# Performance work log

Hardware: AMD Instinct MI355X
Metric: run time of the kernel (lower is better)

Reference implementation:

```python
import jax, jax.numpy as jnp
import numpy as np

HEADS = 8
DIM_HEAD = 64
EPS = 1e-4
SCALE = DIM_HEAD ** -0.5


def setup_inputs() -> dict:
    key = jax.random.key(0)
    k1, k2, k3, k4 = jax.random.split(key, 4)
    dim = HEADS * DIM_HEAD  # 512
    x = jax.random.normal(k1, (2, 2048, dim), dtype=jnp.float32)
    # torch Linear weights are [out, in]; scale like default init
    Wq = jax.random.normal(k2, (dim, dim), dtype=jnp.float32) / np.sqrt(dim)
    Wkv = jax.random.normal(k3, (2 * dim, dim), dtype=jnp.float32) / np.sqrt(dim)
    Wout = jax.random.normal(k4, (dim, dim), dtype=jnp.float32) / np.sqrt(dim)
    return {"x": x, "Wq": Wq, "Wkv": Wkv, "Wout": Wout}


def _normalize_magnitude(t, eps=EPS):
    # divide by (sqrt(mean(t^2, -1)) + eps)
    mag = jnp.sqrt(jnp.mean(t * t, axis=-1, keepdims=True)) + eps
    return t / mag


def reference(x, Wq, Wkv, Wout):
    b, n, dim = x.shape
    h, d = HEADS, DIM_HEAD
    # norm=False -> Identity; context = x (self-attention)
    q = x @ Wq.T                      # [b, n, h*d]
    kv = x @ Wkv.T                    # [b, n, 2*h*d]
    k, v = jnp.split(kv, 2, axis=-1)
    def to_heads(t):
        return t.reshape(b, n, h, d).transpose(0, 2, 1, 3)  # [b, h, n, d]
    q, k, v = map(to_heads, (q, k, v))
    q = _normalize_magnitude(q)
    k = _normalize_magnitude(k)
    sim = jnp.einsum('bhid,bhjd->bhij', q, k) * SCALE
    attn = jax.nn.softmax(sim, axis=-1)
    out = jnp.einsum('bhij,bhjd->bhid', attn, v)
    out = out.transpose(0, 2, 1, 3).reshape(b, n, h * d)
    return out @ Wout.T
```

## Files before the change

### kernel.cpp

```cpp
#include <hip/hip_runtime.h>

typedef __bf16 bf16x8 __attribute__((ext_vector_type(8)));
typedef __bf16 bf16x4 __attribute__((ext_vector_type(4)));
typedef float  f32x4  __attribute__((ext_vector_type(4)));

#define LOG2E_F 1.44269504088896340736f

static constexpr int kB = 2, kN = 2048, kH = 8, kD = 64, kDim = 512;
static constexpr int kTok = kB * kN;
static constexpr int kNQKV = 1536;
static constexpr int kKH = 4;

__device__ __forceinline__ void gld16(const void* g, void* l) {
  __builtin_amdgcn_global_load_lds(
      (const __attribute__((address_space(1))) void*)g,
      (__attribute__((address_space(3))) void*)l, 16, 0, 0);
}


__global__ __launch_bounds__(256) void cvt_all(const float* __restrict__ x,
                                               const float* __restrict__ wq,
                                               const float* __restrict__ wkv,
                                               const float* __restrict__ wo,
                                               __bf16* __restrict__ xb,
                                               __bf16* __restrict__ wqkvb,
                                               __bf16* __restrict__ wob) {
  size_t i = ((size_t)blockIdx.x * 256 + threadIdx.x) * 8;
  const float* s; __bf16* d; size_t off;
  if (i < 2097152)      { s = x;   d = xb;              off = i; }
  else if (i < 2359296) { s = wq;  d = wqkvb;           off = i - 2097152; }
  else if (i < 2883584) { s = wkv; d = wqkvb + 262144;  off = i - 2359296; }
  else                  { s = wo;  d = wob;             off = i - 2883584; }
  float4 u = *(const float4*)(s + off);
  float4 v = *(const float4*)(s + off + 4);
  bf16x8 t;
  t[0] = (__bf16)u.x; t[1] = (__bf16)u.y; t[2] = (__bf16)u.z; t[3] = (__bf16)u.w;
  t[4] = (__bf16)v.x; t[5] = (__bf16)v.y; t[6] = (__bf16)v.z; t[7] = (__bf16)v.w;
  *(bf16x8*)(d + off) = t;
}

__global__ __launch_bounds__(256, 2) void gemm_qkv(const __bf16* __restrict__ A,
                                                   const __bf16* __restrict__ B,
                                                   __bf16* __restrict__ qn,
                                                   __bf16* __restrict__ kn,
                                                   __bf16* __restrict__ vt2) {
  const int K = kDim;
  const int tid = threadIdx.x;
  const int w = tid >> 6, lane = tid & 63, quad = lane >> 4, lq = lane & 15;
  const int m0 = blockIdx.y * 128;
  const int n0 = blockIdx.x * 128;
  const int wm = (w >> 1) * 64, wn = (w & 1) * 64;
  __shared__ __bf16 shm[32768];

  const f32x4 zero = {0.f, 0.f, 0.f, 0.f};
  f32x4 acc[4][4];
#pragma unroll
  for (int fm = 0; fm < 4; ++fm)
#pragma unroll
    for (int fn = 0; fn < 4; ++fn) acc[fm][fn] = zero;

  auto stage = [&](int k0, int buf) {
#pragma unroll
    for (int j = 0; j < 4; ++j) {
      const int s = j * 256 + tid;
      const int row = s >> 3, ch = s & 7;
      const int off = k0 + ((ch ^ (row & 7)) << 3);
      gld16(A + (size_t)(m0 + row) * K + off, &shm[buf * 8192 + s * 8]);
      gld16(B + (size_t)(n0 + row) * K + off, &shm[16384 + buf * 8192 + s * 8]);
    }
  };
  const int sw0 = ((quad ^ (lq & 7)) << 3);
  const int sw1 = (((4 | quad) ^ (lq & 7)) << 3);

  stage(0, 0);
  for (int i = 0; i < 8; ++i) {
    __syncthreads();
    if (i < 7) stage((i + 1) << 6, (i + 1) & 1);
    const int ab = (i & 1) * 8192;
#pragma unroll
    for (int ks = 0; ks < 2; ++ks) {
      const int sw = ks ? sw1 : sw0;
      bf16x8 a[4], b[4];
#pragma unroll
      for (int fm = 0; fm < 4; ++fm)
        a[fm] = *(const bf16x8*)&shm[ab + (wm + fm * 16 + lq) * 64 + sw];
#pragma unroll
      for (int fn = 0; fn < 4; ++fn)
        b[fn] = *(const bf16x8*)&shm[16384 + ab + (wn + fn * 16 + lq) * 64 + sw];
#pragma unroll
      for (int fm = 0; fm < 4; ++fm)
#pragma unroll
        for (int fn = 0; fn < 4; ++fn)
          acc[fm][fn] =
              __builtin_amdgcn_mfma_f32_16x16x32_bf16(a[fm], b[fn], acc[fm][fn], 0, 0, 0);
    }
  }

  const int nb = n0 + wn;
  if (n0 >= 1024) {
    __syncthreads();
    const int hh = wn >> 6;
    const int b = m0 >> 11, kt0 = (m0 & (kN - 1)) >> 6;
#pragma unroll
    for (int fm = 0; fm < 4; ++fm)
#pragma unroll
      for (int r = 0; r < 4; ++r) {
        const int mo = wm + fm * 16 + quad * 4 + r;
        const int rh = mo >> 6, tt = mo & 63;
        const int p = (tt & 15) * 4 + (tt >> 4);
#pragma unroll
        for (int fn = 0; fn < 4; ++fn)
          shm[(hh * 2 + rh) * 4608 + (fn * 16 + lq) * 72 + p] = (__bf16)acc[fm][fn][r];
      }
    __syncthreads();
    const int dd = tid >> 2, p0 = (tid & 3) << 4;
    const int hbase = (n0 >> 6) & 7;
#pragma unroll
    for (int t = 0; t < 4; ++t) {
      const __bf16* src = &shm[t * 4608 + dd * 72 + p0];
      __bf16* dst = vt2 +
          ((size_t)((b * kH + hbase + (t >> 1)) * 32 + kt0 + (t & 1))) * 4096 + tid * 16;
      *(bf16x8*)dst = *(const bf16x8*)src;
      *(bf16x8*)(dst + 8) = *(const bf16x8*)(src + 8);
    }
  } else {
    const int h = (nb >> 6) & 7;
    const float qs = (nb < 512) ? (0.125f * LOG2E_F) : 1.0f;
    __bf16* dst0 = (nb < 512) ? qn : kn;
#pragma unroll
    for (int fm = 0; fm < 4; ++fm)
#pragma unroll
      for (int r = 0; r < 4; ++r) {
        float ss = 0.f;
#pragma unroll
        for (int fn = 0; fn < 4; ++fn) ss += acc[fm][fn][r] * acc[fm][fn][r];
#pragma unroll
        for (int off = 1; off < 16; off <<= 1) ss += __shfl_xor(ss, off, 64);
        const float inv = qs / (sqrtf(ss * (1.f / 64)) + 1e-4f);
        const int m = m0 + wm + fm * 16 + quad * 4 + r;
        const int b = m >> 11, n = m & (kN - 1);
        __bf16* dst = dst0 + ((size_t)(b * kH + h) * kN + n) * kD;
#pragma unroll
        for (int fn = 0; fn < 4; ++fn)
          dst[fn * 16 + lq] = (__bf16)(acc[fm][fn][r] * inv);
      }
  }
}

__global__ __launch_bounds__(256, 2) void attn(const __bf16* __restrict__ qn,
                                               const __bf16* __restrict__ kn,
                                               const __bf16* __restrict__ vt2,
                                               __bf16* __restrict__ po,
                                               float* __restrict__ pl) {
  const int qt = blockIdx.x, bh = blockIdx.y, kh = blockIdx.z;
  const int tid = threadIdx.x;
  const int w = tid >> 6, lane = tid & 63, quad = lane >> 4, lq = lane & 15;
  __shared__ __bf16 Ks[2][4096];
  __shared__ __bf16 Vs[2][4096];
  __shared__ __bf16 Ps[4][64 * 72];
  __bf16* myP = &Ps[w][0];

  bf16x8 aq[4][2];
#pragma unroll
  for (int fm = 0; fm < 4; ++fm) {
    const __bf16* Qb = qn + ((size_t)bh * kN + qt * 256 + w * 64 + fm * 16 + lq) * kD;
    aq[fm][0] = *(const bf16x8*)(Qb + quad * 8);
    aq[fm][1] = *(const bf16x8*)(Qb + 32 + quad * 8);
  }

  const f32x4 zero  = {0.f, 0.f, 0.f, 0.f};
  const f32x4 minit = {-12.f, -12.f, -12.f, -12.f};
  f32x4 o[4][4];
  float lr[4][4];
#pragma unroll
  for (int fm = 0; fm < 4; ++fm)
#pragma unroll
    for (int i = 0; i < 4; ++i) { o[fm][i] = zero; lr[fm][i] = 0.f; }

  const __bf16* Kb = kn + (size_t)bh * kN * kD;
  const __bf16* Vb = vt2 + (size_t)bh * 32 * 4096;

  auto stage = [&](int ktg, int buf) {
#pragma unroll
    for (int j = 0; j < 2; ++j) {
      const int s = j * 256 + tid;
      const int row = s >> 3, ch = s & 7;
      const int src = row * 64 + ((ch ^ (row & 7)) << 3);
      gld16(Kb + (size_t)ktg * 4096 + src, &Ks[buf][s * 8]);
      gld16(Vb + (size_t)ktg * 4096 + src, &Vs[buf][s * 8]);
    }
  };
  const int sw0 = ((quad ^ (lq & 7)) << 3);
  const int sw1 = (((4 | quad) ^ (lq & 7)) << 3);

  const int kt0 = kh * 8;
  stage(kt0, 0);
  for (int kt = 0; kt < 8; ++kt) {
    __syncthreads();
    if (kt < 7) stage(kt0 + kt + 1, (kt + 1) & 1);
    const __bf16* ks_ = &Ks[kt & 1][0];
    const __bf16* vs_ = &Vs[kt & 1][0];

    bf16x8 kb0[4], kb1[4];
#pragma unroll
    for (int fn = 0; fn < 4; ++fn) {
      const int rb = (fn * 16 + lq) * 64;
      kb0[fn] = *(const bf16x8*)&ks_[rb + sw0];
      kb1[fn] = *(const bf16x8*)&ks_[rb + sw1];
    }
#pragma unroll
    for (int fm = 0; fm < 4; ++fm) {
      f32x4 s[4];
#pragma unroll
      for (int fn = 0; fn < 4; ++fn) {
        f32x4 a = __builtin_amdgcn_mfma_f32_16x16x32_bf16(aq[fm][0], kb0[fn], minit, 0, 0, 0);
        s[fn] = __builtin_amdgcn_mfma_f32_16x16x32_bf16(aq[fm][1], kb1[fn], a, 0, 0, 0);
      }
#pragma unroll
      for (int r = 0; r < 4; ++r) {
        const float p0 = __builtin_amdgcn_exp2f(s[0][r]);
        const float p1 = __builtin_amdgcn_exp2f(s[1][r]);
        const float p2 = __builtin_amdgcn_exp2f(s[2][r]);
        const float p3 = __builtin_amdgcn_exp2f(s[3][r]);
        lr[fm][r] += (p0 + p1) + (p2 + p3);
        bf16x4 pk = {(__bf16)p0, (__bf16)p1, (__bf16)p2, (__bf16)p3};
        *(bf16x4*)&myP[(fm * 16 + quad * 4 + r) * 72 + lq * 4] = pk;
      }
    }
    bf16x8 vb0[4], vb1[4];
#pragma unroll
    for (int fn = 0; fn < 4; ++fn) {
      const int rb = (fn * 16 + lq) * 64;
      vb0[fn] = *(const bf16x8*)&vs_[rb + sw0];
      vb1[fn] = *(const bf16x8*)&vs_[rb + sw1];
    }
#pragma unroll
    for (int fm = 0; fm < 4; ++fm) {
      bf16x8 ap0 = *(const bf16x8*)&myP[(fm * 16 + lq) * 72 + quad * 8];
      bf16x8 ap1 = *(const bf16x8*)&myP[(fm * 16 + lq) * 72 + 32 + quad * 8];
#pragma unroll
      for (int fn = 0; fn < 4; ++fn) {
        o[fm][fn] = __builtin_amdgcn_mfma_f32_16x16x32_bf16(ap0, vb0[fn], o[fm][fn], 0, 0, 0);
        o[fm][fn] = __builtin_amdgcn_mfma_f32_16x16x32_bf16(ap1, vb1[fn], o[fm][fn], 0, 0, 0);
      }
    }
  }

  const int b = bh >> 3, h = bh & 7;
#pragma unroll
  for (int fm = 0; fm < 4; ++fm) {
    const int qrow0 = qt * 256 + w * 64 + fm * 16 + quad * 4;
#pragma unroll
    for (int r = 0; r < 4; ++r) {
      float sum = lr[fm][r];
#pragma unroll
      for (int off = 1; off < 16; off <<= 1) sum += __shfl_xor(sum, off, 64);
      if (lq == 0) pl[(size_t)kh * 32768 + bh * kN + qrow0 + r] = sum;
      const size_t ob = ((size_t)kh * kTok + b * kN + qrow0 + r) * kDim + h * 64;
#pragma unroll
      for (int fn = 0; fn < 4; ++fn) po[ob + fn * 16 + lq] = (__bf16)o[fm][fn][r];
    }
  }
}

__global__ __launch_bounds__(256) void combine(const __bf16* __restrict__ po,
                                               const float* __restrict__ pl,
                                               __bf16* __restrict__ ao) {
  const size_t i = ((size_t)blockIdx.x * 256 + threadIdx.x) * 4;
  const int tok = (int)(i >> 9), dk = (int)(i & 511);
  const int h = dk >> 6, b = tok >> 11, qrow = tok & (kN - 1);
  const int idx = (b * kH + h) * kN + qrow;
  float l = 0.f;
#pragma unroll
  for (int kh = 0; kh < kKH; ++kh) l += pl[kh * 32768 + idx];
  const float inv = 1.f / l;
  float s0 = 0.f, s1 = 0.f, s2 = 0.f, s3 = 0.f;
#pragma unroll
  for (int kh = 0; kh < kKH; ++kh) {
    bf16x4 a = *(const bf16x4*)(po + (size_t)kh * kTok * kDim + i);
    s0 += (float)a[0]; s1 += (float)a[1]; s2 += (float)a[2]; s3 += (float)a[3];
  }
  bf16x4 t = {(__bf16)(s0 * inv), (__bf16)(s1 * inv),
              (__bf16)(s2 * inv), (__bf16)(s3 * inv)};
  *(bf16x4*)(ao + i) = t;
}

__global__ __launch_bounds__(256, 2) void gemm64(const __bf16* __restrict__ A,
                                                 const __bf16* __restrict__ B,
                                                 float* __restrict__ C,
                                                 int N, int K) {
  const int tid = threadIdx.x;
  const int w = tid >> 6, lane = tid & 63, quad = lane >> 4, lq = lane & 15;
  const int m0 = blockIdx.y * 64;
  const int n0 = blockIdx.x * 64;
  const int wm = (w >> 1) * 32, wn = (w & 1) * 32;
  __shared__ __bf16 As[2][4096];
  __shared__ __bf16 Bs[2][4096];

  const f32x4 zero = {0.f, 0.f, 0.f, 0.f};
  f32x4 acc00 = zero, acc01 = zero, acc10 = zero, acc11 = zero;

  const int sr = tid >> 3, ch = tid & 7;
  auto stage = [&](int k0, int buf) {
#pragma unroll
    for (int j = 0; j < 2; ++j) {
      const int row = j * 32 + sr;
      const int src = k0 + ((ch ^ (row & 7)) << 3);
      gld16(A + (size_t)(m0 + row) * K + src, &As[buf][row * 64 + ch * 8]);
      gld16(B + (size_t)(n0 + row) * K + src, &Bs[buf][row * 64 + ch * 8]);
    }
  };
  const int sw0 = ((quad ^ (lq & 7)) << 3);
  const int sw1 = (((4 | quad) ^ (lq & 7)) << 3);

  stage(0, 0);
  const int iters = K >> 6;
  for (int i = 0; i < iters; ++i) {
    __syncthreads();
    if (i + 1 < iters) stage((i + 1) << 6, (i + 1) & 1);
    const __bf16* as = &As[i & 1][0];
    const __bf16* bs = &Bs[i & 1][0];
#pragma unroll
    for (int ks = 0; ks < 2; ++ks) {
      const int sw = ks ? sw1 : sw0;
      bf16x8 a0 = *(const bf16x8*)&as[(wm +      lq) * 64 + sw];
      bf16x8 a1 = *(const bf16x8*)&as[(wm + 16 + lq) * 64 + sw];
      bf16x8 b0 = *(const bf16x8*)&bs[(wn +      lq) * 64 + sw];
      bf16x8 b1 = *(const bf16x8*)&bs[(wn + 16 + lq) * 64 + sw];
      acc00 = __builtin_amdgcn_mfma_f32_16x16x32_bf16(a0, b0, acc00, 0, 0, 0);
      acc01 = __builtin_amdgcn_mfma_f32_16x16x32_bf16(a0, b1, acc01, 0, 0, 0);
      acc10 = __builtin_amdgcn_mfma_f32_16x16x32_bf16(a1, b0, acc10, 0, 0, 0);
      acc11 = __builtin_amdgcn_mfma_f32_16x16x32_bf16(a1, b1, acc11, 0, 0, 0);
    }
  }
  const f32x4 av[2][2] = {{acc00, acc01}, {acc10, acc11}};
#pragma unroll
  for (int fm = 0; fm < 2; ++fm)
#pragma unroll
    for (int fn = 0; fn < 2; ++fn)
#pragma unroll
      for (int r = 0; r < 4; ++r)
        C[(size_t)(m0 + wm + fm * 16 + quad * 4 + r) * N + (n0 + wn + fn * 16 + lq)] =
            av[fm][fn][r];
}

extern "C" void kernel_launch(void* const* d_in, const int* in_sizes, int n_in,
                              void* d_out, int out_size, void* d_ws, size_t ws_size,
                              hipStream_t stream) {
  const float* x    = (const float*)d_in[0];
  const float* Wq   = (const float*)d_in[1];
  const float* Wkv  = (const float*)d_in[2];
  const float* Wout = (const float*)d_in[3];
  float* out = (float*)d_out;
  char* ws = (char*)d_ws;

  __bf16* xb    = (__bf16*)(ws);
  __bf16* wqkvb = (__bf16*)(ws + (size_t)(4 << 20));
  __bf16* wob   = (__bf16*)(ws + (size_t)(6 << 20));
  __bf16* qn    = (__bf16*)(ws + (size_t)(7 << 20));
  __bf16* kn    = (__bf16*)(ws + (size_t)(11 << 20));
  __bf16* vt2   = (__bf16*)(ws + (size_t)(15 << 20));
  __bf16* po    = (__bf16*)(ws + (size_t)(19 << 20));
  float*  pl    = (float*)(ws + (size_t)(35 << 20));
  __bf16* ao    = (__bf16*)(ws + (size_t)(36 << 20));

  cvt_all<<<1536, 256, 0, stream>>>(x, Wq, Wkv, Wout, xb, wqkvb, wob);
  gemm_qkv<<<dim3(kNQKV / 128, kTok / 128), 256, 0, stream>>>(xb, wqkvb, qn, kn, vt2);
  attn<<<dim3(kN / 256, kB * kH, kKH), 256, 0, stream>>>(qn, kn, vt2, po, pl);
  combine<<<kTok * kDim / 1024, 256, 0, stream>>>(po, pl, ao);
  gemm64<<<dim3(kDim / 64, kTok / 64), 256, 0, stream>>>(ao, wob, out, kDim, kDim);
}
```

Measured before the change: 118.9 us.

## Fuse split-KV combine into output GEMM and retile attention to 2-way split

The split-KV combine kernel is removed. The output projection GEMM now loads both partial attention outputs, sums them, normalizes by the summed row sums, and writes the bf16 A tile to shared memory itself, which drops one launch and the intermediate buffer round trip. Attention now uses 2 KV splits with 128-query blocks (32 rows per wave) and occupancy hint 3, so each block runs a longer loop with fewer registers. The trade-off is that A-tile staging in the GEMM becomes synchronous register loads with arithmetic, where before it was an async global-to-LDS copy.

```diff
diff --git a/kernel.cpp b/kernel.cpp
--- a/kernel.cpp
+++ b/kernel.cpp
@@ -9,7 +9,7 @@
 static constexpr int kB = 2, kN = 2048, kH = 8, kD = 64, kDim = 512;
 static constexpr int kTok = kB * kN;
 static constexpr int kNQKV = 1536;
-static constexpr int kKH = 4;
+static constexpr int kKH = 2;
 
 __device__ __forceinline__ void gld16(const void* g, void* l) {
   __builtin_amdgcn_global_load_lds(
@@ -147,7 +147,7 @@
   }
 }
 
-__global__ __launch_bounds__(256, 2) void attn(const __bf16* __restrict__ qn,
+__global__ __launch_bounds__(256, 3) void attn(const __bf16* __restrict__ qn,
                                                const __bf16* __restrict__ kn,
                                                const __bf16* __restrict__ vt2,
                                                __bf16* __restrict__ po,
@@ -157,23 +157,23 @@
   const int w = tid >> 6, lane = tid & 63, quad = lane >> 4, lq = lane & 15;
   __shared__ __bf16 Ks[2][4096];
   __shared__ __bf16 Vs[2][4096];
-  __shared__ __bf16 Ps[4][64 * 72];
+  __shared__ __bf16 Ps[4][32 * 72];
   __bf16* myP = &Ps[w][0];
 
-  bf16x8 aq[4][2];
-#pragma unroll
-  for (int fm = 0; fm < 4; ++fm) {
-    const __bf16* Qb = qn + ((size_t)bh * kN + qt * 256 + w * 64 + fm * 16 + lq) * kD;
+  bf16x8 aq[2][2];
+#pragma unroll
+  for (int fm = 0; fm < 2; ++fm) {
+    const __bf16* Qb = qn + ((size_t)bh * kN + qt * 128 + w * 32 + fm * 16 + lq) * kD;
     aq[fm][0] = *(const bf16x8*)(Qb + quad * 8);
     aq[fm][1] = *(const bf16x8*)(Qb + 32 + quad * 8);
   }
 
   const f32x4 zero  = {0.f, 0.f, 0.f, 0.f};
   const f32x4 minit = {-12.f, -12.f, -12.f, -12.f};
-  f32x4 o[4][4];
-  float lr[4][4];
-#pragma unroll
-  for (int fm = 0; fm < 4; ++fm)
+  f32x4 o[2][4];
+  float lr[2][4];
+#pragma unroll
+  for (int fm = 0; fm < 2; ++fm)
 #pragma unroll
     for (int i = 0; i < 4; ++i) { o[fm][i] = zero; lr[fm][i] = 0.f; }
 
@@ -193,49 +193,47 @@
   const int sw0 = ((quad ^ (lq & 7)) << 3);
   const int sw1 = (((4 | quad) ^ (lq & 7)) << 3);
 
-  const int kt0 = kh * 8;
+  const int kt0 = kh * 16;
   stage(kt0, 0);
-  for (int kt = 0; kt < 8; ++kt) {
-    __syncthreads();
-    if (kt < 7) stage(kt0 + kt + 1, (kt + 1) & 1);
+  for (int kt = 0; kt < 16; ++kt) {
+    __syncthreads();
+    if (kt < 15) stage(kt0 + kt + 1, (kt + 1) & 1);
     const __bf16* ks_ = &Ks[kt & 1][0];
     const __bf16* vs_ = &Vs[kt & 1][0];
 
-    bf16x8 kb0[4], kb1[4];
+    bf16x8 kb0[4], kb1[4], vb0[4], vb1[4];
 #pragma unroll
     for (int fn = 0; fn < 4; ++fn) {
       const int rb = (fn * 16 + lq) * 64;
       kb0[fn] = *(const bf16x8*)&ks_[rb + sw0];
       kb1[fn] = *(const bf16x8*)&ks_[rb + sw1];
-    }
-#pragma unroll
-    for (int fm = 0; fm < 4; ++fm) {
-      f32x4 s[4];
+      vb0[fn] = *(const bf16x8*)&vs_[rb + sw0];
+      vb1[fn] = *(const bf16x8*)&vs_[rb + sw1];
+    }
+    f32x4 s[2][4];
+#pragma unroll
+    for (int fm = 0; fm < 2; ++fm)
 #pragma unroll
       for (int fn = 0; fn < 4; ++fn) {
         f32x4 a = __builtin_amdgcn_mfma_f32_16x16x32_bf16(aq[fm][0], kb0[fn], minit, 0, 0, 0);
-        s[fn] = __builtin_amdgcn_mfma_f32_16x16x32_bf16(aq[fm][1], kb1[fn], a, 0, 0, 0);
-      }
+        s[fm][fn] = __builtin_amdgcn_mfma_f32_16x16x32_bf16(aq[fm][1], kb1[fn], a, 0, 0, 0);
+      }
+
+#pragma unroll
+    for (int fm = 0; fm < 2; ++fm)
 #pragma unroll
       for (int r = 0; r < 4; ++r) {
-        const float p0 = __builtin_amdgcn_exp2f(s[0][r]);
-        const float p1 = __builtin_amdgcn_exp2f(s[1][r]);
-        const float p2 = __builtin_amdgcn_exp2f(s[2][r]);
-        const float p3 = __builtin_amdgcn_exp2f(s[3][r]);
+        const float p0 = __builtin_amdgcn_exp2f(s[fm][0][r]);
+        const float p1 = __builtin_amdgcn_exp2f(s[fm][1][r]);
+        const float p2 = __builtin_amdgcn_exp2f(s[fm][2][r]);
+        const float p3 = __builtin_amdgcn_exp2f(s[fm][3][r]);
         lr[fm][r] += (p0 + p1) + (p2 + p3);
         bf16x4 pk = {(__bf16)p0, (__bf16)p1, (__bf16)p2, (__bf16)p3};
         *(bf16x4*)&myP[(fm * 16 + quad * 4 + r) * 72 + lq * 4] = pk;
       }
-    }
-    bf16x8 vb0[4], vb1[4];
-#pragma unroll
-    for (int fn = 0; fn < 4; ++fn) {
-      const int rb = (fn * 16 + lq) * 64;
-      vb0[fn] = *(const bf16x8*)&vs_[rb + sw0];
-      vb1[fn] = *(const bf16x8*)&vs_[rb + sw1];
-    }
-#pragma unroll
-    for (int fm = 0; fm < 4; ++fm) {
+
+#pragma unroll
+    for (int fm = 0; fm < 2; ++fm) {
       bf16x8 ap0 = *(const bf16x8*)&myP[(fm * 16 + lq) * 72 + quad * 8];
       bf16x8 ap1 = *(const bf16x8*)&myP[(fm * 16 + lq) * 72 + 32 + quad * 8];
 #pragma unroll
@@ -248,8 +246,8 @@
 
   const int b = bh >> 3, h = bh & 7;
 #pragma unroll
-  for (int fm = 0; fm < 4; ++fm) {
-    const int qrow0 = qt * 256 + w * 64 + fm * 16 + quad * 4;
+  for (int fm = 0; fm < 2; ++fm) {
+    const int qrow0 = qt * 128 + w * 32 + fm * 16 + quad * 4;
 #pragma unroll
     for (int r = 0; r < 4; ++r) {
       float sum = lr[fm][r];
@@ -263,32 +261,11 @@
   }
 }
 
-__global__ __launch_bounds__(256) void combine(const __bf16* __restrict__ po,
-                                               const float* __restrict__ pl,
-                                               __bf16* __restrict__ ao) {
-  const size_t i = ((size_t)blockIdx.x * 256 + threadIdx.x) * 4;
-  const int tok = (int)(i >> 9), dk = (int)(i & 511);
-  const int h = dk >> 6, b = tok >> 11, qrow = tok & (kN - 1);
-  const int idx = (b * kH + h) * kN + qrow;
-  float l = 0.f;
-#pragma unroll
-  for (int kh = 0; kh < kKH; ++kh) l += pl[kh * 32768 + idx];
-  const float inv = 1.f / l;
-  float s0 = 0.f, s1 = 0.f, s2 = 0.f, s3 = 0.f;
-#pragma unroll
-  for (int kh = 0; kh < kKH; ++kh) {
-    bf16x4 a = *(const bf16x4*)(po + (size_t)kh * kTok * kDim + i);
-    s0 += (float)a[0]; s1 += (float)a[1]; s2 += (float)a[2]; s3 += (float)a[3];
-  }
-  bf16x4 t = {(__bf16)(s0 * inv), (__bf16)(s1 * inv),
-              (__bf16)(s2 * inv), (__bf16)(s3 * inv)};
-  *(bf16x4*)(ao + i) = t;
-}
-
-__global__ __launch_bounds__(256, 2) void gemm64(const __bf16* __restrict__ A,
-                                                 const __bf16* __restrict__ B,
-                                                 float* __restrict__ C,
-                                                 int N, int K) {
+__global__ __launch_bounds__(256, 2) void gemm_out(const __bf16* __restrict__ po,
+                                                   const float* __restrict__ pl,
+                                                   const __bf16* __restrict__ B,
+                                                   float* __restrict__ C) {
+  const int N = kDim, K = kDim;
   const int tid = threadIdx.x;
   const int w = tid >> 6, lane = tid & 63, quad = lane >> 4, lq = lane & 15;
   const int m0 = blockIdx.y * 64;
@@ -301,23 +278,41 @@
   f32x4 acc00 = zero, acc01 = zero, acc10 = zero, acc11 = zero;
 
   const int sr = tid >> 3, ch = tid & 7;
-  auto stage = [&](int k0, int buf) {
+  auto stageA = [&](int i, int buf) {
+#pragma unroll
+    for (int j = 0; j < 2; ++j) {
+      const int row = j * 32 + sr;
+      const int m = m0 + row;
+      const int chs = ch ^ (row & 7);
+      const size_t base = (size_t)m * K + i * 64 + chs * 8;
+      bf16x8 a0 = *(const bf16x8*)(po + base);
+      bf16x8 a1 = *(const bf16x8*)(po + (size_t)kTok * kDim + base);
+      const int bb = m >> 11, qrow = m & (kN - 1);
+      const int idx = (bb * kH + i) * kN + qrow;
+      const float inv = 1.f / (pl[idx] + pl[32768 + idx]);
+      bf16x8 t;
+#pragma unroll
+      for (int e = 0; e < 8; ++e)
+        t[e] = (__bf16)(((float)a0[e] + (float)a1[e]) * inv);
+      *(bf16x8*)&As[buf][row * 64 + ch * 8] = t;
+    }
+  };
+  auto stageB = [&](int k0, int buf) {
 #pragma unroll
     for (int j = 0; j < 2; ++j) {
       const int row = j * 32 + sr;
       const int src = k0 + ((ch ^ (row & 7)) << 3);
-      gld16(A + (size_t)(m0 + row) * K + src, &As[buf][row * 64 + ch * 8]);
       gld16(B + (size_t)(n0 + row) * K + src, &Bs[buf][row * 64 + ch * 8]);
     }
   };
   const int sw0 = ((quad ^ (lq & 7)) << 3);
   const int sw1 = (((4 | quad) ^ (lq & 7)) << 3);
 
-  stage(0, 0);
-  const int iters = K >> 6;
-  for (int i = 0; i < iters; ++i) {
-    __syncthreads();
-    if (i + 1 < iters) stage((i + 1) << 6, (i + 1) & 1);
+  stageB(0, 0);
+  stageA(0, 0);
+  for (int i = 0; i < 8; ++i) {
+    __syncthreads();
+    if (i + 1 < 8) { stageB((i + 1) << 6, (i + 1) & 1); stageA(i + 1, (i + 1) & 1); }
     const __bf16* as = &As[i & 1][0];
     const __bf16* bs = &Bs[i & 1][0];
 #pragma unroll
@@ -361,12 +356,10 @@
   __bf16* kn    = (__bf16*)(ws + (size_t)(11 << 20));
   __bf16* vt2   = (__bf16*)(ws + (size_t)(15 << 20));
   __bf16* po    = (__bf16*)(ws + (size_t)(19 << 20));
-  float*  pl    = (float*)(ws + (size_t)(35 << 20));
-  __bf16* ao    = (__bf16*)(ws + (size_t)(36 << 20));
+  float*  pl    = (float*)(ws + (size_t)(27 << 20));
 
   cvt_all<<<1536, 256, 0, stream>>>(x, Wq, Wkv, Wout, xb, wqkvb, wob);
   gemm_qkv<<<dim3(kNQKV / 128, kTok / 128), 256, 0, stream>>>(xb, wqkvb, qn, kn, vt2);
-  attn<<<dim3(kN / 256, kB * kH, kKH), 256, 0, stream>>>(qn, kn, vt2, po, pl);
-  combine<<<kTok * kDim / 1024, 256, 0, stream>>>(po, pl, ao);
-  gemm64<<<dim3(kDim / 64, kTok / 64), 256, 0, stream>>>(ao, wob, out, kDim, kDim);
-}
+  attn<<<dim3(kN / 128, kB * kH, kKH), 256, 0, stream>>>(qn, kn, vt2, po, pl);
+  gemm_out<<<dim3(kDim / 64, kTok / 64), 256, 0, stream>>>(po, pl, wob, out);
+}
```

New measurement: 122.2 us. +2.7%, slower.
